# Kernel optimization log

Measured on AMD Instinct MI355X. Metric: run time of the kernel, lower is better.

The kernel has to match this reference:

```python
import jax, jax.numpy as jnp
import numpy as np

N_NODES = 50000
N_EDGES = 800000
IN_FEATS = 256
OUT_FEATS = 64


def setup_inputs() -> dict:
    key = jax.random.key(0)
    k1, k2, k3, k4, k5 = jax.random.split(key, 5)
    feat = jax.random.normal(k1, (N_NODES, IN_FEATS), dtype=jnp.float32)
    weight = jax.random.normal(k2, (OUT_FEATS, IN_FEATS), dtype=jnp.float32) * (1.0 / np.sqrt(IN_FEATS))
    bias = jax.random.normal(k3, (OUT_FEATS,), dtype=jnp.float32) * 0.01
    src = jax.random.randint(k4, (N_EDGES,), 0, N_NODES, dtype=jnp.int32)
    dst = jax.random.randint(k5, (N_EDGES,), 0, N_NODES, dtype=jnp.int32)
    return {"feat": feat, "weight": weight, "bias": bias, "src": src, "dst": dst}


def reference(feat, weight, bias, src, dst):
    # GCN conv, norm='both', in_feats > out_feats branch:
    #   feat := feat * out_deg^{-1/2}; h := feat @ W^T (Qlinear); rst := SpMM(copy_u,sum);
    #   rst := rst * in_deg^{-1/2} + bias
    n = feat.shape[0]
    ones = jnp.ones(src.shape, dtype=jnp.float32)
    out_deg = jnp.clip(jax.ops.segment_sum(ones, src, num_segments=n), 1.0)  # [N]
    in_deg = jnp.clip(jax.ops.segment_sum(ones, dst, num_segments=n), 1.0)   # [N]

    h = feat * jax.lax.rsqrt(out_deg)[:, None]          # left norm
    h = jnp.einsum('ni,oi->no', h, weight)              # [N, out] quantized linear (fp math)
    msg = jnp.take(h, src, axis=0)                      # gather: copy_u, [E, out]
    rst = jax.ops.segment_sum(msg, dst, num_segments=n) # scatter-sum, [N, out]
    rst = rst * jax.lax.rsqrt(in_deg)[:, None]          # right norm
    rst = rst + bias
    return rst
```

## Files before the change

### kernel.cpp

```cpp
#include <hip/hip_runtime.h>
#include <hip/hip_bf16.h>


#define IN_F 256
#define OUT_F 64
#define CAP 64

typedef short bf16x8 __attribute__((ext_vector_type(8)));
typedef float f32x4 __attribute__((ext_vector_type(4)));
typedef unsigned short u16x8 __attribute__((ext_vector_type(8)));

static __host__ __device__ inline size_t ws_align(size_t x) { return (x + 15) & ~(size_t)15; }

__device__ inline unsigned short f2bf(float x) {
  unsigned u = __float_as_uint(x);
  unsigned r = (u + 0x7fffu + ((u >> 16) & 1u)) >> 16;
  return (unsigned short)r;
}
__device__ inline float bf2f(unsigned short b) { return __uint_as_float(((unsigned)b) << 16); }

__global__ void fill2_kernel(const int* __restrict__ src, const int* __restrict__ dst,
                             int* __restrict__ outcnt, int* __restrict__ cursor,
                             unsigned short* __restrict__ csr, int E) {
  int e = blockIdx.x * blockDim.x + threadIdx.x;
  if (e < E) {
    int s = src[e], d = dst[e];
    atomicAdd(&outcnt[s], 1);
    int p = atomicAdd(&cursor[d], 1);
    csr[(size_t)d * CAP + p] = (unsigned short)s;
  }
}

__global__ void wsplit_kernel(const float* __restrict__ W, unsigned short* __restrict__ whi,
                              unsigned short* __restrict__ wlo, int total) {
  int i = blockIdx.x * blockDim.x + threadIdx.x;
  if (i < total) {
    float x = W[i];
    unsigned short hb = f2bf(x);
    whi[i] = hb;
    wlo[i] = f2bf(x - bf2f(hb));
  }
}

__global__ __launch_bounds__(256) void gemm_kernel(const float* __restrict__ feat,
                                                   const unsigned short* __restrict__ whi,
                                                   const unsigned short* __restrict__ wlo,
                                                   const int* __restrict__ outcnt,
                                                   float* __restrict__ h, int n) {
  const int tid = threadIdx.x;
  const int wave = tid >> 6;
  const int lane = tid & 63;
  const int lrow = lane & 15;
  const int kgrp = lane >> 4;
  const int base = blockIdx.x * 64 + wave * 16;

  f32x4 acc[4] = {};

  int anode = base + lrow;
  if (anode >= n) anode = n - 1;
  const float* ap = feat + (size_t)anode * IN_F + kgrp * 8;
  const int wofs = lrow * IN_F + kgrp * 8;

#pragma unroll 2
  for (int k0 = 0; k0 < IN_F; k0 += 32) {
    float4 a0 = *(const float4*)(ap + k0);
    float4 a1 = *(const float4*)(ap + k0 + 4);
    float av[8] = {a0.x, a0.y, a0.z, a0.w, a1.x, a1.y, a1.z, a1.w};
    bf16x8 fhi, flo;
#pragma unroll
    for (int j = 0; j < 8; ++j) {
      unsigned short hb = f2bf(av[j]);
      fhi[j] = (short)hb;
      flo[j] = (short)f2bf(av[j] - bf2f(hb));
    }
#pragma unroll
    for (int oj = 0; oj < 4; ++oj) {
      const int bofs = oj * 16 * IN_F + wofs + k0;
      bf16x8 bhi = *(const bf16x8*)(whi + bofs);
      bf16x8 blo = *(const bf16x8*)(wlo + bofs);
      acc[oj] = __builtin_amdgcn_mfma_f32_16x16x32_bf16(fhi, bhi, acc[oj], 0, 0, 0);
      acc[oj] = __builtin_amdgcn_mfma_f32_16x16x32_bf16(fhi, blo, acc[oj], 0, 0, 0);
      acc[oj] = __builtin_amdgcn_mfma_f32_16x16x32_bf16(flo, bhi, acc[oj], 0, 0, 0);
    }
  }

#pragma unroll
  for (int r = 0; r < 4; ++r) {
    int node = base + kgrp * 4 + r;
    if (node < n) {
      float rs = 1.0f / sqrtf(fmaxf((float)outcnt[node], 1.0f));
#pragma unroll
      for (int oj = 0; oj < 4; ++oj) {
        h[(size_t)node * OUT_F + oj * 16 + lrow] = acc[oj][r] * rs;
      }
    }
  }
}

__global__ __launch_bounds__(256) void gather_kernel(const float* __restrict__ h,
                                                     const int* __restrict__ cursor,
                                                     const unsigned short* __restrict__ csr,
                                                     const float* __restrict__ bias,
                                                     float* __restrict__ out, int n) {
  int node = (blockIdx.x * blockDim.x + threadIdx.x) >> 6;
  int lane = threadIdx.x & 63;
  if (node >= n) return;
  int cnt = cursor[node];
  const unsigned short* bp = csr + (size_t)node * CAP;
  float acc = 0.f;
  int p = 0;
  for (; p + 8 <= cnt; p += 8) {
    u16x8 v = *(const u16x8*)(bp + p);
    float a0 = h[(size_t)v[0] * OUT_F + lane], a1 = h[(size_t)v[1] * OUT_F + lane];
    float a2 = h[(size_t)v[2] * OUT_F + lane], a3 = h[(size_t)v[3] * OUT_F + lane];
    float a4 = h[(size_t)v[4] * OUT_F + lane], a5 = h[(size_t)v[5] * OUT_F + lane];
    float a6 = h[(size_t)v[6] * OUT_F + lane], a7 = h[(size_t)v[7] * OUT_F + lane];
    acc += ((a0 + a1) + (a2 + a3)) + ((a4 + a5) + (a6 + a7));
  }
  for (; p < cnt; ++p) acc += h[(size_t)bp[p] * OUT_F + lane];
  float rs = 1.0f / sqrtf(fmaxf((float)cnt, 1.0f));
  out[(size_t)node * OUT_F + lane] = acc * rs + bias[lane];
}

extern "C" void kernel_launch(void* const* d_in, const int* in_sizes, int n_in,
                              void* d_out, int out_size, void* d_ws, size_t ws_size,
                              hipStream_t stream) {
  const float* feat = (const float*)d_in[0];
  const float* W    = (const float*)d_in[1];
  const float* bias = (const float*)d_in[2];
  const int* src    = (const int*)d_in[3];
  const int* dst    = (const int*)d_in[4];
  float* out = (float*)d_out;

  const int N = in_sizes[0] / IN_F;
  const int E = in_sizes[3];
  const int WTOT = OUT_F * IN_F;

  size_t o_outcnt = 0;
  size_t o_cursor = o_outcnt + ws_align(N);
  size_t o_csr    = o_cursor + ws_align(N);
  size_t o_whi    = o_csr + ws_align((size_t)N * CAP / 2);
  size_t o_wlo    = o_whi + ws_align(WTOT / 2);
  size_t o_h      = o_wlo + ws_align(WTOT / 2);

  int* outcnt  = (int*)d_ws + o_outcnt;
  int* cursor  = (int*)d_ws + o_cursor;
  unsigned short* csr = (unsigned short*)((int*)d_ws + o_csr);
  unsigned short* whi = (unsigned short*)((int*)d_ws + o_whi);
  unsigned short* wlo = (unsigned short*)((int*)d_ws + o_wlo);
  float* h     = (float*)d_ws + o_h;

  hipMemsetAsync(d_ws, 0, o_csr * sizeof(int), stream);

  int eb = (E + 255) / 256;
  wsplit_kernel<<<(WTOT + 255) / 256, 256, 0, stream>>>(W, whi, wlo, WTOT);
  fill2_kernel<<<eb, 256, 0, stream>>>(src, dst, outcnt, cursor, csr, E);
  gemm_kernel<<<(N + 63) / 64, 256, 0, stream>>>(feat, whi, wlo, outcnt, h, N);
  gather_kernel<<<(N + 3) / 4, 256, 0, stream>>>(h, cursor, csr, bias, out, N);
}
```

Before: 234.9 us.

## Fuse edge CSR fill into GEMM launch and move out-degree norm into gather

Merges the edge-fill kernel and the GEMM into one launch, with extra blocks beyond the GEMM range doing atomic degree counting and CSR fill, so the two independent stages can overlap on the GPU. Because the GEMM no longer waits for out-degree counts, the left normalization moves into the gather kernel, which now loads outcnt per source edge and scales each message. This removes a kernel boundary and lets atomic-bound fill work run alongside the compute-bound GEMM. The cost is eight extra random outcnt loads plus reciprocal square roots per gathered edge group.

```diff
diff --git a/kernel.cpp b/kernel.cpp
--- a/kernel.cpp
+++ b/kernel.cpp
@@ -19,18 +19,6 @@
 }
 __device__ inline float bf2f(unsigned short b) { return __uint_as_float(((unsigned)b) << 16); }
 
-__global__ void fill2_kernel(const int* __restrict__ src, const int* __restrict__ dst,
-                             int* __restrict__ outcnt, int* __restrict__ cursor,
-                             unsigned short* __restrict__ csr, int E) {
-  int e = blockIdx.x * blockDim.x + threadIdx.x;
-  if (e < E) {
-    int s = src[e], d = dst[e];
-    atomicAdd(&outcnt[s], 1);
-    int p = atomicAdd(&cursor[d], 1);
-    csr[(size_t)d * CAP + p] = (unsigned short)s;
-  }
-}
-
 __global__ void wsplit_kernel(const float* __restrict__ W, unsigned short* __restrict__ whi,
                               unsigned short* __restrict__ wlo, int total) {
   int i = blockIdx.x * blockDim.x + threadIdx.x;
@@ -42,11 +30,26 @@
   }
 }
 
-__global__ __launch_bounds__(256) void gemm_kernel(const float* __restrict__ feat,
-                                                   const unsigned short* __restrict__ whi,
-                                                   const unsigned short* __restrict__ wlo,
-                                                   const int* __restrict__ outcnt,
-                                                   float* __restrict__ h, int n) {
+__global__ __launch_bounds__(256) void fused_kernel(const float* __restrict__ feat,
+                                                    const unsigned short* __restrict__ whi,
+                                                    const unsigned short* __restrict__ wlo,
+                                                    const int* __restrict__ src,
+                                                    const int* __restrict__ dst,
+                                                    int* __restrict__ outcnt,
+                                                    int* __restrict__ cursor,
+                                                    unsigned short* __restrict__ csr,
+                                                    float* __restrict__ h,
+                                                    int n, int E, int gemmBlocks) {
+  if ((int)blockIdx.x >= gemmBlocks) {
+    int e = ((int)blockIdx.x - gemmBlocks) * 256 + threadIdx.x;
+    if (e < E) {
+      int s = src[e], d = dst[e];
+      atomicAdd(&outcnt[s], 1);
+      int p = atomicAdd(&cursor[d], 1);
+      csr[(size_t)d * CAP + p] = (unsigned short)s;
+    }
+    return;
+  }
   const int tid = threadIdx.x;
   const int wave = tid >> 6;
   const int lane = tid & 63;
@@ -88,10 +91,9 @@
   for (int r = 0; r < 4; ++r) {
     int node = base + kgrp * 4 + r;
     if (node < n) {
-      float rs = 1.0f / sqrtf(fmaxf((float)outcnt[node], 1.0f));
 #pragma unroll
       for (int oj = 0; oj < 4; ++oj) {
-        h[(size_t)node * OUT_F + oj * 16 + lrow] = acc[oj][r] * rs;
+        h[(size_t)node * OUT_F + oj * 16 + lrow] = acc[oj][r];
       }
     }
   }
@@ -99,6 +101,7 @@
 
 __global__ __launch_bounds__(256) void gather_kernel(const float* __restrict__ h,
                                                      const int* __restrict__ cursor,
+                                                     const int* __restrict__ outcnt,
                                                      const unsigned short* __restrict__ csr,
                                                      const float* __restrict__ bias,
                                                      float* __restrict__ out, int n) {
@@ -111,13 +114,28 @@
   int p = 0;
   for (; p + 8 <= cnt; p += 8) {
     u16x8 v = *(const u16x8*)(bp + p);
-    float a0 = h[(size_t)v[0] * OUT_F + lane], a1 = h[(size_t)v[1] * OUT_F + lane];
-    float a2 = h[(size_t)v[2] * OUT_F + lane], a3 = h[(size_t)v[3] * OUT_F + lane];
-    float a4 = h[(size_t)v[4] * OUT_F + lane], a5 = h[(size_t)v[5] * OUT_F + lane];
-    float a6 = h[(size_t)v[6] * OUT_F + lane], a7 = h[(size_t)v[7] * OUT_F + lane];
-    acc += ((a0 + a1) + (a2 + a3)) + ((a4 + a5) + (a6 + a7));
+    int s0 = v[0], s1 = v[1], s2 = v[2], s3 = v[3];
+    int s4 = v[4], s5 = v[5], s6 = v[6], s7 = v[7];
+    float r0 = 1.0f / sqrtf(fmaxf((float)outcnt[s0], 1.0f));
+    float r1 = 1.0f / sqrtf(fmaxf((float)outcnt[s1], 1.0f));
+    float r2 = 1.0f / sqrtf(fmaxf((float)outcnt[s2], 1.0f));
+    float r3 = 1.0f / sqrtf(fmaxf((float)outcnt[s3], 1.0f));
+    float r4 = 1.0f / sqrtf(fmaxf((float)outcnt[s4], 1.0f));
+    float r5 = 1.0f / sqrtf(fmaxf((float)outcnt[s5], 1.0f));
+    float r6 = 1.0f / sqrtf(fmaxf((float)outcnt[s6], 1.0f));
+    float r7 = 1.0f / sqrtf(fmaxf((float)outcnt[s7], 1.0f));
+    float a0 = h[(size_t)s0 * OUT_F + lane], a1 = h[(size_t)s1 * OUT_F + lane];
+    float a2 = h[(size_t)s2 * OUT_F + lane], a3 = h[(size_t)s3 * OUT_F + lane];
+    float a4 = h[(size_t)s4 * OUT_F + lane], a5 = h[(size_t)s5 * OUT_F + lane];
+    float a6 = h[(size_t)s6 * OUT_F + lane], a7 = h[(size_t)s7 * OUT_F + lane];
+    acc += ((a0 * r0 + a1 * r1) + (a2 * r2 + a3 * r3)) +
+           ((a4 * r4 + a5 * r5) + (a6 * r6 + a7 * r7));
   }
-  for (; p < cnt; ++p) acc += h[(size_t)bp[p] * OUT_F + lane];
+  for (; p < cnt; ++p) {
+    int s = bp[p];
+    float r = 1.0f / sqrtf(fmaxf((float)outcnt[s], 1.0f));
+    acc += h[(size_t)s * OUT_F + lane] * r;
+  }
   float rs = 1.0f / sqrtf(fmaxf((float)cnt, 1.0f));
   out[(size_t)node * OUT_F + lane] = acc * rs + bias[lane];
 }
@@ -152,9 +170,11 @@
 
   hipMemsetAsync(d_ws, 0, o_csr * sizeof(int), stream);
 
-  int eb = (E + 255) / 256;
+  const int gemmBlocks = (N + 63) / 64;
+  const int fillBlocks = (E + 255) / 256;
   wsplit_kernel<<<(WTOT + 255) / 256, 256, 0, stream>>>(W, whi, wlo, WTOT);
-  fill2_kernel<<<eb, 256, 0, stream>>>(src, dst, outcnt, cursor, csr, E);
-  gemm_kernel<<<(N + 63) / 64, 256, 0, stream>>>(feat, whi, wlo, outcnt, h, N);
-  gather_kernel<<<(N + 3) / 4, 256, 0, stream>>>(h, cursor, csr, bias, out, N);
+  fused_kernel<<<gemmBlocks + fillBlocks, 256, 0, stream>>>(feat, whi, wlo, src, dst,
+                                                            outcnt, cursor, csr, h,
+                                                            N, E, gemmBlocks);
+  gather_kernel<<<(N + 3) / 4, 256, 0, stream>>>(h, cursor, outcnt, csr, bias, out, N);
 }
```

Measured after the change: 231.6 us. About the same (-1.4%).
